# Kernel tuning notes

Measured on AMD Instinct MI355X. Metric: run time of the kernel, lower is better.

The kernel has to match this reference:

```python
import jax, jax.numpy as jnp
import numpy as np

N_NODES = 100000
N_EDGES = 640000
D = 128
L = 3


def setup_inputs() -> dict:
    key = jax.random.key(0)
    k1, k2, k3 = jax.random.split(key, 3)
    x = jax.random.normal(k1, (N_NODES, D), dtype=jnp.float32)
    edge_index = jax.random.randint(k2, (2, N_EDGES), 0, N_NODES, dtype=jnp.int64)
    batch = jnp.zeros((N_NODES,), dtype=jnp.int64)
    W = jax.random.normal(k3, (L, D, D), dtype=jnp.float32) / np.sqrt(D)
    b = jnp.zeros((L, D), dtype=jnp.float32)
    return {"x": x, "edge_index": edge_index, "batch": batch, "W": W, "b": b}


def _gcn_forward(x, edge_index, W, b):
    row, col = edge_index[0], edge_index[1]  # source, target
    n = x.shape[0]
    # symmetric normalization (PyG gcn_norm, add_self_loops=False, unit edge weights)
    deg = jax.ops.segment_sum(jnp.ones((row.shape[0],), dtype=x.dtype), col, num_segments=n)
    dinv = jnp.where(deg > 0, jax.lax.rsqrt(jnp.where(deg > 0, deg, 1.0)), 0.0)
    norm = dinv[row] * dinv[col]  # [E]
    for i in range(W.shape[0]):
        h = x @ W[i]                                   # [N, D]
        msg = h[row] * norm[:, None]                   # gather + scale, [E, D]
        x = jax.ops.segment_sum(msg, col, num_segments=n) + b[i]
        if i < W.shape[0] - 1:
            x = jax.nn.relu(x)
    return x


def reference(x, edge_index, batch, W, b):
    return _gcn_forward(x, edge_index, W, b)
```

## Files before the change

### kernel.cpp

```cpp
#include <hip/hip_runtime.h>
#include <math.h>

#define NN 100000
#define NE 640000
#define DD 128
#define LSTRIDE 132
#define SLOT_CAP 32

typedef __attribute__((ext_vector_type(8))) short short8;
typedef __attribute__((ext_vector_type(4))) float floatx4;

static const size_t OFF_DEG    = 0;
static const size_t OFF_GCTR   = 400000;
static const size_t OFF_DINV   = 400064;
static const size_t OFF_OFF    = 800064;
static const size_t OFF_CURSOR = 1200064;
static const size_t OFF_WHP    = 1600064;
static const size_t OFF_WLP    = 1698368;
static const size_t OFF_EIDX   = 1796672;
static const size_t OFF_H_FB   = 4357120;
static const size_t OFF_SLOT   = 4356864;
static const size_t OFF_H_SL   = 17157120;
static const size_t WS_NEED_SL = 17157120 + (size_t)NN * DD * 4;
static const size_t WS_NEED_FB = 4357120 + (size_t)NN * DD * 4;

__device__ __forceinline__ unsigned bf16_rne(float f) {
    unsigned u = __float_as_uint(f);
    return (u + 0x7FFFu + ((u >> 16) & 1u)) >> 16;
}

__device__ __forceinline__ void pack_W(int t, const float* __restrict__ W,
                                       ushort* __restrict__ Whp,
                                       ushort* __restrict__ Wlp) {
    if (t < 3 * 2048) {
        int l = t >> 11;
        int r = t & 2047;
        int kc = r >> 9;
        int nt = (r >> 6) & 7;
        int L  = r & 63;
        int n  = nt * 16 + (L & 15);
        int k0 = kc * 32 + (L >> 4) * 8;
        const float* Wl_ = W + (size_t)l * DD * DD;
        size_t base = ((size_t)l * 2048 + r) * 8;
        #pragma unroll
        for (int j = 0; j < 8; ++j) {
            float f = Wl_[(size_t)(k0 + j) * DD + n];
            unsigned hi = bf16_rne(f);
            float fh = __uint_as_float(hi << 16);
            unsigned lo = bf16_rne(f - fh);
            Whp[base + j] = (ushort)hi;
            Wlp[base + j] = (ushort)lo;
        }
    }
}

__global__ __launch_bounds__(256) void fill_slots_pack(const int* __restrict__ rowi,
                                                       const int* __restrict__ coli,
                                                       int* __restrict__ cnt,
                                                       int* __restrict__ slot,
                                                       const float* __restrict__ W,
                                                       ushort* __restrict__ Whp,
                                                       ushort* __restrict__ Wlp) {
    int t = blockIdx.x * 256 + threadIdx.x;
    int e0 = t * 4;
    if (e0 < NE) {
        int4 s4 = *(const int4*)(rowi + e0);
        int4 d4 = *(const int4*)(coli + e0);
        int p0 = atomicAdd(&cnt[d4.x], 1);
        int p1 = atomicAdd(&cnt[d4.y], 1);
        int p2 = atomicAdd(&cnt[d4.z], 1);
        int p3 = atomicAdd(&cnt[d4.w], 1);
        if (p0 < SLOT_CAP) slot[(d4.x << 5) + p0] = s4.x;
        if (p1 < SLOT_CAP) slot[(d4.y << 5) + p1] = s4.y;
        if (p2 < SLOT_CAP) slot[(d4.z << 5) + p2] = s4.z;
        if (p3 < SLOT_CAP) slot[(d4.w << 5) + p3] = s4.w;
    }
    pack_W(t, W, Whp, Wlp);
}

__global__ __launch_bounds__(256) void finish_setup(int* __restrict__ cnt,
                                                    float* __restrict__ dinv) {
    int i = blockIdx.x * 256 + threadIdx.x;
    if (i < NN) {
        int d = cnt[i];
        if (d > SLOT_CAP) { d = SLOT_CAP; cnt[i] = d; }
        dinv[i] = (d > 0) ? 1.0f / sqrtf((float)d) : 0.0f;
    }
}

__global__ __launch_bounds__(256) void count_and_pack(const int* __restrict__ coli,
                                                      int* __restrict__ deg,
                                                      const float* __restrict__ W,
                                                      ushort* __restrict__ Whp,
                                                      ushort* __restrict__ Wlp) {
    int e = blockIdx.x * 256 + threadIdx.x;
    if (e < NE) atomicAdd(&deg[coli[e]], 1);
    pack_W(e, W, Whp, Wlp);
}

__global__ __launch_bounds__(256) void alloc_offsets(const int* __restrict__ deg,
                                                     int* __restrict__ off,
                                                     int* __restrict__ cursor,
                                                     float* __restrict__ dinv,
                                                     unsigned* __restrict__ gctr) {
    int i = blockIdx.x * 256 + threadIdx.x;
    int v = (i < NN) ? deg[i] : 0;
    if (i < NN) dinv[i] = (v > 0) ? 1.0f / sqrtf((float)v) : 0.0f;

    int lane = threadIdx.x & 63;
    int sv = v;
    #pragma unroll
    for (int s = 1; s < 64; s <<= 1) {
        int t = __shfl_up(sv, s, 64);
        if (lane >= s) sv += t;
    }
    int wtot = __shfl(sv, 63, 64);
    int base = 0;
    if (lane == 63) base = (int)atomicAdd(gctr, (unsigned)wtot);
    base = __shfl(base, 63, 64);
    int o = base + sv - v;
    if (i < NN) {
        off[i] = o;
        cursor[i] = o;
    }
}

__global__ __launch_bounds__(256) void fill_csr(const int* __restrict__ rowi,
                                                const int* __restrict__ coli,
                                                int* __restrict__ cursor,
                                                int* __restrict__ eidx) {
    int e = blockIdx.x * 256 + threadIdx.x;
    if (e < NE) {
        int s = rowi[e], d = coli[e];
        int pos = atomicAdd(&cursor[d], 1);
        eidx[pos] = s;
    }
}

template<int MODE, bool SLOTS>
__global__ __launch_bounds__(256) void fused_layer(
        const float* __restrict__ Xin,
        const ushort* __restrict__ Whp,
        const ushort* __restrict__ Wlp,
        const int* __restrict__ off,
        const int* __restrict__ deg,
        const int* __restrict__ eidx,
        const float* __restrict__ dinv,
        const float* __restrict__ bias,
        float* __restrict__ Y) {
    __shared__ float Ls[32 * LSTRIDE];
    int tid = threadIdx.x;
    int n0 = blockIdx.x * 32;

    {
        int g = tid >> 5, lane = tid & 31;
        int c0 = lane * 4;
        #pragma unroll
        for (int t = 0; t < 4; ++t) {
            int nl = g * 4 + t;
            int node = n0 + nl;
            float4 a0 = make_float4(0.f, 0.f, 0.f, 0.f);
            float4 a1 = a0, a2 = a0, a3 = a0;
            if (node < NN) {
                int s = SLOTS ? (node << 5) : off[node];
                int e = s + deg[node];
                for (int j = s; j < e; j += 4) {
                    int j1 = j + 1, j2 = j + 2, j3 = j + 3;
                    int s0, s1, s2, s3;
                    if (SLOTS) {
                        int4 q4 = *(const int4*)(eidx + j);
                        s0 = q4.x;
                        s1 = (j1 < e) ? q4.y : 0;
                        s2 = (j2 < e) ? q4.z : 0;
                        s3 = (j3 < e) ? q4.w : 0;
                    } else {
                        int i1 = (j1 < e) ? j1 : j;
                        int i2 = (j2 < e) ? j2 : j;
                        int i3 = (j3 < e) ? j3 : j;
                        s0 = eidx[j];  s1 = eidx[i1];
                        s2 = eidx[i2]; s3 = eidx[i3];
                    }
                    float w0, w1, w2, w3;
                    if (MODE == 0) {
                        w0 = dinv[s0];
                        w1 = (j1 < e) ? dinv[s1] : 0.f;
                        w2 = (j2 < e) ? dinv[s2] : 0.f;
                        w3 = (j3 < e) ? dinv[s3] : 0.f;
                    } else {
                        w0 = 1.f;
                        w1 = (j1 < e) ? 1.f : 0.f;
                        w2 = (j2 < e) ? 1.f : 0.f;
                        w3 = (j3 < e) ? 1.f : 0.f;
                    }
                    float4 v0 = *(const float4*)(Xin + (size_t)s0 * DD + c0);
                    float4 v1 = *(const float4*)(Xin + (size_t)s1 * DD + c0);
                    float4 v2 = *(const float4*)(Xin + (size_t)s2 * DD + c0);
                    float4 v3 = *(const float4*)(Xin + (size_t)s3 * DD + c0);
                    a0.x = fmaf(w0, v0.x, a0.x); a0.y = fmaf(w0, v0.y, a0.y);
                    a0.z = fmaf(w0, v0.z, a0.z); a0.w = fmaf(w0, v0.w, a0.w);
                    a1.x = fmaf(w1, v1.x, a1.x); a1.y = fmaf(w1, v1.y, a1.y);
                    a1.z = fmaf(w1, v1.z, a1.z); a1.w = fmaf(w1, v1.w, a1.w);
                    a2.x = fmaf(w2, v2.x, a2.x); a2.y = fmaf(w2, v2.y, a2.y);
                    a2.z = fmaf(w2, v2.z, a2.z); a2.w = fmaf(w2, v2.w, a2.w);
                    a3.x = fmaf(w3, v3.x, a3.x); a3.y = fmaf(w3, v3.y, a3.y);
                    a3.z = fmaf(w3, v3.z, a3.z); a3.w = fmaf(w3, v3.w, a3.w);
                }
            }
            float4 r = make_float4((a0.x + a1.x) + (a2.x + a3.x),
                                   (a0.y + a1.y) + (a2.y + a3.y),
                                   (a0.z + a1.z) + (a2.z + a3.z),
                                   (a0.w + a1.w) + (a2.w + a3.w));
            *(float4*)(&Ls[nl * LSTRIDE + c0]) = r;
        }
    }
    __syncthreads();

    int wave = tid >> 6;
    int lane = tid & 63;
    int m    = lane & 15;
    int quad = lane >> 4;
    int mt   = wave >> 1;
    int nh   = (wave & 1) * 4;

    floatx4 acc[4];
    #pragma unroll
    for (int q = 0; q < 4; ++q) acc[q] = (floatx4){0.f, 0.f, 0.f, 0.f};

    #pragma unroll
    for (int kc = 0; kc < 4; ++kc) {
        const float* lp = &Ls[(mt * 16 + m) * LSTRIDE + kc * 32 + quad * 8];
        float4 xa = *(const float4*)(lp);
        float4 xb = *(const float4*)(lp + 4);
        float xs[8] = {xa.x, xa.y, xa.z, xa.w, xb.x, xb.y, xb.z, xb.w};
        short8 ah, al;
        #pragma unroll
        for (int j = 0; j < 8; ++j) {
            unsigned hi = bf16_rne(xs[j]);
            float fh = __uint_as_float(hi << 16);
            unsigned lo = bf16_rne(xs[j] - fh);
            ah[j] = (short)hi;
            al[j] = (short)lo;
        }
        #pragma unroll
        for (int q = 0; q < 4; ++q) {
            int nt = nh + q;
            size_t fidx = (((size_t)(kc * 8 + nt)) * 64 + lane) * 8;
            short8 bh = *(const short8*)(Whp + fidx);
            short8 bl = *(const short8*)(Wlp + fidx);
            acc[q] = __builtin_amdgcn_mfma_f32_16x16x32_bf16(al, bh, acc[q], 0, 0, 0);
            acc[q] = __builtin_amdgcn_mfma_f32_16x16x32_bf16(ah, bl, acc[q], 0, 0, 0);
            acc[q] = __builtin_amdgcn_mfma_f32_16x16x32_bf16(ah, bh, acc[q], 0, 0, 0);
        }
    }

    #pragma unroll
    for (int i = 0; i < 4; ++i) {
        int ro = n0 + mt * 16 + quad * 4 + i;
        if (ro < NN) {
            float s = dinv[ro];
            float s2 = s * s;
            #pragma unroll
            for (int q = 0; q < 4; ++q) {
                int col = (nh + q) * 16 + m;
                float v;
                if (MODE < 2) {
                    v = fmaf(acc[q][i], s2, bias[col] * s);
                    v = fmaxf(v, 0.f);
                } else {
                    v = fmaf(acc[q][i], s, bias[col]);
                }
                Y[(size_t)ro * DD + col] = v;
            }
        }
    }
}


extern "C" void kernel_launch(void* const* d_in, const int* in_sizes, int n_in,
                              void* d_out, int out_size, void* d_ws, size_t ws_size,
                              hipStream_t stream) {
    const float* x  = (const float*)d_in[0];
    const int*   ei = (const int*)d_in[1];
    const float* W  = (const float*)d_in[3];
    const float* b  = (const float*)d_in[4];
    float* out = (float*)d_out;

    char* ws = (char*)d_ws;
    int*      deg    = (int*)(ws + OFF_DEG);
    unsigned* gctr   = (unsigned*)(ws + OFF_GCTR);
    float*    dinv   = (float*)(ws + OFF_DINV);
    int*      off    = (int*)(ws + OFF_OFF);
    int*      cursor = (int*)(ws + OFF_CURSOR);
    ushort*   whp    = (ushort*)(ws + OFF_WHP);
    ushort*   wlp    = (ushort*)(ws + OFF_WLP);

    const int* rowi = ei;
    const int* coli = ei + NE;

    int nblk = (NN + 31) / 32;

    if (ws_size >= WS_NEED_SL) {
        int*   slot = (int*)(ws + OFF_SLOT);
        float* H    = (float*)(ws + OFF_H_SL);
        hipMemsetAsync(ws + OFF_DEG, 0, 400000, stream);
        fill_slots_pack<<<(NE / 4 + 255) / 256, 256, 0, stream>>>(rowi, coli, deg, slot,
                                                                  W, whp, wlp);
        finish_setup<<<(NN + 255) / 256, 256, 0, stream>>>(deg, dinv);

        fused_layer<0, true><<<nblk, 256, 0, stream>>>(x,   whp,         wlp,
                                                       nullptr, deg, slot, dinv, b,          out);
        fused_layer<1, true><<<nblk, 256, 0, stream>>>(out, whp + 16384, wlp + 16384,
                                                       nullptr, deg, slot, dinv, b + DD,     H);
        fused_layer<2, true><<<nblk, 256, 0, stream>>>(H,   whp + 32768, wlp + 32768,
                                                       nullptr, deg, slot, dinv, b + 2 * DD, out);
    } else {
        int*   eidx = (int*)(ws + OFF_EIDX);
        float* H    = (float*)(ws + OFF_H_FB);
        hipMemsetAsync(ws, 0, 400064, stream);
        count_and_pack<<<(NE + 255) / 256, 256, 0, stream>>>(coli, deg, W, whp, wlp);
        alloc_offsets<<<(NN + 255) / 256, 256, 0, stream>>>(deg, off, cursor, dinv, gctr);
        fill_csr<<<(NE + 255) / 256, 256, 0, stream>>>(rowi, coli, cursor, eidx);

        fused_layer<0, false><<<nblk, 256, 0, stream>>>(x,   whp,         wlp,
                                                        off, deg, eidx, dinv, b,          out);
        fused_layer<1, false><<<nblk, 256, 0, stream>>>(out, whp + 16384, wlp + 16384,
                                                        off, deg, eidx, dinv, b + DD,     H);
        fused_layer<2, false><<<nblk, 256, 0, stream>>>(H,   whp + 32768, wlp + 32768,
                                                        off, deg, eidx, dinv, b + 2 * DD, out);
    }
}
```

Measured before the change: 331.6 us.

## Restructure slot gather to one wave per 8 nodes with shuffled indices

The slot-path aggregation now assigns each wave 8 nodes, and each lane covers 2 feature columns across all 128. Each lane loads its slice of the slot index row once and broadcasts indices with wave shuffles, so 8 neighbor rows are gathered per iteration instead of 4. The goal is more memory-level parallelism and fewer redundant index and degree loads. Bounds checks are dropped because the node count divides evenly by 32, which ties correctness to that constant. Slots beyond 32 per node are not handled.

```diff
diff --git a/kernel.cpp b/kernel.cpp
--- a/kernel.cpp
+++ b/kernel.cpp
@@ -137,8 +137,142 @@
     }
 }
 
-template<int MODE, bool SLOTS>
-__global__ __launch_bounds__(256) void fused_layer(
+template<int MODE>
+__device__ __forceinline__ void mfma_phase(const float* __restrict__ Ls,
+                                           const ushort* __restrict__ Whp,
+                                           const ushort* __restrict__ Wlp,
+                                           const float* __restrict__ dinv,
+                                           const float* __restrict__ bias,
+                                           float* __restrict__ Y,
+                                           int n0, int tid) {
+    int wave = tid >> 6;
+    int lane = tid & 63;
+    int m    = lane & 15;
+    int quad = lane >> 4;
+    int mt   = wave >> 1;
+    int nh   = (wave & 1) * 4;
+
+    floatx4 acc[4];
+    #pragma unroll
+    for (int q = 0; q < 4; ++q) acc[q] = (floatx4){0.f, 0.f, 0.f, 0.f};
+
+    #pragma unroll
+    for (int kc = 0; kc < 4; ++kc) {
+        const float* lp = &Ls[(mt * 16 + m) * LSTRIDE + kc * 32 + quad * 8];
+        float4 xa = *(const float4*)(lp);
+        float4 xb = *(const float4*)(lp + 4);
+        float xs[8] = {xa.x, xa.y, xa.z, xa.w, xb.x, xb.y, xb.z, xb.w};
+        short8 ah, al;
+        #pragma unroll
+        for (int j = 0; j < 8; ++j) {
+            unsigned hi = bf16_rne(xs[j]);
+            float fh = __uint_as_float(hi << 16);
+            unsigned lo = bf16_rne(xs[j] - fh);
+            ah[j] = (short)hi;
+            al[j] = (short)lo;
+        }
+        #pragma unroll
+        for (int q = 0; q < 4; ++q) {
+            int nt = nh + q;
+            size_t fidx = (((size_t)(kc * 8 + nt)) * 64 + lane) * 8;
+            short8 bh = *(const short8*)(Whp + fidx);
+            short8 bl = *(const short8*)(Wlp + fidx);
+            acc[q] = __builtin_amdgcn_mfma_f32_16x16x32_bf16(al, bh, acc[q], 0, 0, 0);
+            acc[q] = __builtin_amdgcn_mfma_f32_16x16x32_bf16(ah, bl, acc[q], 0, 0, 0);
+            acc[q] = __builtin_amdgcn_mfma_f32_16x16x32_bf16(ah, bh, acc[q], 0, 0, 0);
+        }
+    }
+
+    #pragma unroll
+    for (int i = 0; i < 4; ++i) {
+        int ro = n0 + mt * 16 + quad * 4 + i;
+        float s = dinv[ro];
+        float s2 = s * s;
+        #pragma unroll
+        for (int q = 0; q < 4; ++q) {
+            int col = (nh + q) * 16 + m;
+            float v;
+            if (MODE < 2) {
+                v = fmaf(acc[q][i], s2, bias[col] * s);
+                v = fmaxf(v, 0.f);
+            } else {
+                v = fmaf(acc[q][i], s, bias[col]);
+            }
+            Y[(size_t)ro * DD + col] = v;
+        }
+    }
+}
+
+template<int MODE>
+__global__ __launch_bounds__(256) void fused_layer_slots(
+        const float* __restrict__ Xin,
+        const ushort* __restrict__ Whp,
+        const ushort* __restrict__ Wlp,
+        const int* __restrict__ deg,
+        const int* __restrict__ slot,
+        const float* __restrict__ dinv,
+        const float* __restrict__ bias,
+        float* __restrict__ Y) {
+    __shared__ float Ls[32 * LSTRIDE];
+    int tid  = threadIdx.x;
+    int n0   = blockIdx.x * 32;
+    int wave = tid >> 6, lane = tid & 63;
+
+    int nbase = n0 + wave * 8;
+    int4 srow = *(const int4*)(slot + nbase * 32 + lane * 4);
+    int  d8   = deg[nbase + (lane & 7)];
+    int  c0   = lane * 2;
+
+    #pragma unroll 1
+    for (int nl = 0; nl < 8; ++nl) {
+        int d = __shfl(d8, nl, 64);
+        float2 acc = make_float2(0.f, 0.f);
+        for (int j0 = 0; j0 < d; j0 += 8) {
+            int rem = d - j0;
+            int idx[8];
+            #pragma unroll
+            for (int k = 0; k < 8; ++k) {
+                int owner = nl * 8 + (j0 >> 2) + (k >> 2);
+                int e;
+                switch (k & 3) {
+                    case 0:  e = srow.x; break;
+                    case 1:  e = srow.y; break;
+                    case 2:  e = srow.z; break;
+                    default: e = srow.w; break;
+                }
+                e = __shfl(e, owner, 64);
+                idx[k] = (k < rem) ? e : 0;
+            }
+            float w[8];
+            if (MODE == 0) {
+                #pragma unroll
+                for (int k = 0; k < 8; ++k) {
+                    float t = dinv[idx[k]];
+                    w[k] = (k < rem) ? t : 0.f;
+                }
+            } else {
+                #pragma unroll
+                for (int k = 0; k < 8; ++k) w[k] = (k < rem) ? 1.f : 0.f;
+            }
+            float2 v[8];
+            #pragma unroll
+            for (int k = 0; k < 8; ++k)
+                v[k] = *(const float2*)(Xin + (size_t)idx[k] * DD + c0);
+            #pragma unroll
+            for (int k = 0; k < 8; ++k) {
+                acc.x = fmaf(w[k], v[k].x, acc.x);
+                acc.y = fmaf(w[k], v[k].y, acc.y);
+            }
+        }
+        *(float2*)(&Ls[(wave * 8 + nl) * LSTRIDE + c0]) = acc;
+    }
+    __syncthreads();
+
+    mfma_phase<MODE>(Ls, Whp, Wlp, dinv, bias, Y, n0, tid);
+}
+
+template<int MODE>
+__global__ __launch_bounds__(256) void fused_layer_csr(
         const float* __restrict__ Xin,
         const ushort* __restrict__ Whp,
         const ushort* __restrict__ Wlp,
@@ -151,7 +285,6 @@
     __shared__ float Ls[32 * LSTRIDE];
     int tid = threadIdx.x;
     int n0 = blockIdx.x * 32;
-
     {
         int g = tid >> 5, lane = tid & 31;
         int c0 = lane * 4;
@@ -161,25 +294,16 @@
             int node = n0 + nl;
             float4 a0 = make_float4(0.f, 0.f, 0.f, 0.f);
             float4 a1 = a0, a2 = a0, a3 = a0;
-            if (node < NN) {
-                int s = SLOTS ? (node << 5) : off[node];
+            {
+                int s = off[node];
                 int e = s + deg[node];
                 for (int j = s; j < e; j += 4) {
                     int j1 = j + 1, j2 = j + 2, j3 = j + 3;
-                    int s0, s1, s2, s3;
-                    if (SLOTS) {
-                        int4 q4 = *(const int4*)(eidx + j);
-                        s0 = q4.x;
-                        s1 = (j1 < e) ? q4.y : 0;
-                        s2 = (j2 < e) ? q4.z : 0;
-                        s3 = (j3 < e) ? q4.w : 0;
-                    } else {
-                        int i1 = (j1 < e) ? j1 : j;
-                        int i2 = (j2 < e) ? j2 : j;
-                        int i3 = (j3 < e) ? j3 : j;
-                        s0 = eidx[j];  s1 = eidx[i1];
-                        s2 = eidx[i2]; s3 = eidx[i3];
-                    }
+                    int i1 = (j1 < e) ? j1 : j;
+                    int i2 = (j2 < e) ? j2 : j;
+                    int i3 = (j3 < e) ? j3 : j;
+                    int s0 = eidx[j],  s1 = eidx[i1];
+                    int s2 = eidx[i2], s3 = eidx[i3];
                     float w0, w1, w2, w3;
                     if (MODE == 0) {
                         w0 = dinv[s0];
@@ -214,65 +338,7 @@
         }
     }
     __syncthreads();
-
-    int wave = tid >> 6;
-    int lane = tid & 63;
-    int m    = lane & 15;
-    int quad = lane >> 4;
-    int mt   = wave >> 1;
-    int nh   = (wave & 1) * 4;
-
-    floatx4 acc[4];
-    #pragma unroll
-    for (int q = 0; q < 4; ++q) acc[q] = (floatx4){0.f, 0.f, 0.f, 0.f};
-
-    #pragma unroll
-    for (int kc = 0; kc < 4; ++kc) {
-        const float* lp = &Ls[(mt * 16 + m) * LSTRIDE + kc * 32 + quad * 8];
-        float4 xa = *(const float4*)(lp);
-        float4 xb = *(const float4*)(lp + 4);
-        float xs[8] = {xa.x, xa.y, xa.z, xa.w, xb.x, xb.y, xb.z, xb.w};
-        short8 ah, al;
-        #pragma unroll
-        for (int j = 0; j < 8; ++j) {
-            unsigned hi = bf16_rne(xs[j]);
-            float fh = __uint_as_float(hi << 16);
-            unsigned lo = bf16_rne(xs[j] - fh);
-            ah[j] = (short)hi;
-            al[j] = (short)lo;
-        }
-        #pragma unroll
-        for (int q = 0; q < 4; ++q) {
-            int nt = nh + q;
-            size_t fidx = (((size_t)(kc * 8 + nt)) * 64 + lane) * 8;
-            short8 bh = *(const short8*)(Whp + fidx);
-            short8 bl = *(const short8*)(Wlp + fidx);
-            acc[q] = __builtin_amdgcn_mfma_f32_16x16x32_bf16(al, bh, acc[q], 0, 0, 0);
-            acc[q] = __builtin_amdgcn_mfma_f32_16x16x32_bf16(ah, bl, acc[q], 0, 0, 0);
-            acc[q] = __builtin_amdgcn_mfma_f32_16x16x32_bf16(ah, bh, acc[q], 0, 0, 0);
-        }
-    }
-
-    #pragma unroll
-    for (int i = 0; i < 4; ++i) {
-        int ro = n0 + mt * 16 + quad * 4 + i;
-        if (ro < NN) {
-            float s = dinv[ro];
-            float s2 = s * s;
-            #pragma unroll
-            for (int q = 0; q < 4; ++q) {
-                int col = (nh + q) * 16 + m;
-                float v;
-                if (MODE < 2) {
-                    v = fmaf(acc[q][i], s2, bias[col] * s);
-                    v = fmaxf(v, 0.f);
-                } else {
-                    v = fmaf(acc[q][i], s, bias[col]);
-                }
-                Y[(size_t)ro * DD + col] = v;
-            }
-        }
-    }
+    mfma_phase<MODE>(Ls, Whp, Wlp, dinv, bias, Y, n0, tid);
 }
 
 
@@ -297,7 +363,7 @@
     const int* rowi = ei;
     const int* coli = ei + NE;
 
-    int nblk = (NN + 31) / 32;
+    int nblk = NN / 32;
 
     if (ws_size >= WS_NEED_SL) {
         int*   slot = (int*)(ws + OFF_SLOT);
@@ -307,12 +373,12 @@
                                                                   W, whp, wlp);
         finish_setup<<<(NN + 255) / 256, 256, 0, stream>>>(deg, dinv);
 
-        fused_layer<0, true><<<nblk, 256, 0, stream>>>(x,   whp,         wlp,
-                                                       nullptr, deg, slot, dinv, b,          out);
-        fused_layer<1, true><<<nblk, 256, 0, stream>>>(out, whp + 16384, wlp + 16384,
-                                                       nullptr, deg, slot, dinv, b + DD,     H);
-        fused_layer<2, true><<<nblk, 256, 0, stream>>>(H,   whp + 32768, wlp + 32768,
-                                                       nullptr, deg, slot, dinv, b + 2 * DD, out);
+        fused_layer_slots<0><<<nblk, 256, 0, stream>>>(x,   whp,         wlp,
+                                                       deg, slot, dinv, b,          out);
+        fused_layer_slots<1><<<nblk, 256, 0, stream>>>(out, whp + 16384, wlp + 16384,
+                                                       deg, slot, dinv, b + DD,     H);
+        fused_layer_slots<2><<<nblk, 256, 0, stream>>>(H,   whp + 32768, wlp + 32768,
+                                                       deg, slot, dinv, b + 2 * DD, out);
     } else {
         int*   eidx = (int*)(ws + OFF_EIDX);
         float* H    = (float*)(ws + OFF_H_FB);
@@ -321,11 +387,11 @@
         alloc_offsets<<<(NN + 255) / 256, 256, 0, stream>>>(deg, off, cursor, dinv, gctr);
         fill_csr<<<(NE + 255) / 256, 256, 0, stream>>>(rowi, coli, cursor, eidx);
 
-        fused_layer<0, false><<<nblk, 256, 0, stream>>>(x,   whp,         wlp,
-                                                        off, deg, eidx, dinv, b,          out);
-        fused_layer<1, false><<<nblk, 256, 0, stream>>>(out, whp + 16384, wlp + 16384,
-                                                        off, deg, eidx, dinv, b + DD,     H);
-        fused_layer<2, false><<<nblk, 256, 0, stream>>>(H,   whp + 32768, wlp + 32768,
-                                                        off, deg, eidx, dinv, b + 2 * DD, out);
-    }
-}
+        fused_layer_csr<0><<<nblk, 256, 0, stream>>>(x,   whp,         wlp,
+                                                     off, deg, eidx, dinv, b,          out);
+        fused_layer_csr<1><<<nblk, 256, 0, stream>>>(out, whp + 16384, wlp + 16384,
+                                                     off, deg, eidx, dinv, b + DD,     H);
+        fused_layer_csr<2><<<nblk, 256, 0, stream>>>(H,   whp + 32768, wlp + 32768,
+                                                     off, deg, eidx, dinv, b + 2 * DD, out);
+    }
+}
```

After: 310.6 us. 6.3% less time.
